# Kernel optimization log

Hardware: AMD Instinct MI355X
Metric: run time of the kernel (lower is better)

## Reference

```python
import jax, jax.numpy as jnp
import numpy as np


def setup_inputs() -> dict:
    key = jax.random.key(0)
    ks = jax.random.split(key, 9)
    bs, nf, h, w = 4, 512, 64, 64
    c8 = nf // 8
    sc = 1.0 / np.sqrt(nf)
    return {
        "x": jax.random.normal(ks[0], (bs, nf, h, w), dtype=jnp.float32),
        "Wq": jax.random.normal(ks[1], (c8, nf), dtype=jnp.float32) * sc,
        "bq": jax.random.normal(ks[2], (c8,), dtype=jnp.float32) * 0.01,
        "Wk": jax.random.normal(ks[3], (c8, nf), dtype=jnp.float32) * sc,
        "bk": jax.random.normal(ks[4], (c8,), dtype=jnp.float32) * 0.01,
        "Wv": jax.random.normal(ks[5], (nf, nf), dtype=jnp.float32) * sc,
        "bv": jax.random.normal(ks[6], (nf,), dtype=jnp.float32) * 0.01,
        "alpha": jax.random.normal(ks[7], (1,), dtype=jnp.float32) * 0.1,
    }


def reference(x, Wq, bq, Wk, bk, Wv, bv, alpha):
    bs, nf, h, w = x.shape
    hw = h * w
    xf = x.reshape(bs, nf, hw)  # flatten spatial; 1x1 conv == channel matmul
    q = jnp.einsum('oc,bcn->bon', Wq, xf) + bq[:, None]  # (bs, c8, hw)
    k = jnp.einsum('oc,bcn->bon', Wk, xf) + bk[:, None]  # (bs, c8, hw)
    v = jnp.einsum('oc,bcn->bon', Wv, xf) + bv[:, None]  # (bs, nf, hw)
    # scores[b, i, j] = key_i . query_j ; softmax over j (queries)
    scores = jnp.einsum('bci,bcj->bij', k, q)  # (bs, hw, hw)
    attn = jax.nn.softmax(scores, axis=-1)
    # out[b, c, i] = sum_j v[b, c, j] * attn[b, i, j]
    out = jnp.einsum('bcj,bij->bci', v, attn).reshape(bs, nf, h, w)
    return x + alpha * out
```

## Files before the change

### kernel.cpp

```cpp
#include <hip/hip_runtime.h>

#define BS 4
#define NF 512
#define HW 4096
#define C8 64
#define TI 64

typedef unsigned short bfu;
typedef __attribute__((ext_vector_type(8))) short bf16x8;
typedef __attribute__((ext_vector_type(4))) float f32x4;

static __device__ __forceinline__ bfu f2bu(float v) {
    union { unsigned int u; float f; } c; c.f = v;
    unsigned int u = c.u;
    u = u + 0x7FFFu + ((u >> 16) & 1u);
    return (bfu)(u >> 16);
}

static __device__ __forceinline__ unsigned int cvt_pk_bf16(float lo, float hi) {
    unsigned int r;
    asm("v_cvt_pk_bf16_f32 %0, %1, %2" : "=v"(r) : "v"(lo), "v"(hi));
    return r;
}

static __device__ __forceinline__ void gload16(const void* g, void* l) {
    __builtin_amdgcn_global_load_lds(
        (const __attribute__((address_space(1))) unsigned int*)g,
        (__attribute__((address_space(3))) unsigned int*)l,
        16, 0, 0);
}

__global__ __launch_bounds__(256) void k0_xt(const float* __restrict__ x, bfu* __restrict__ xt)
{
    __shared__ float T[64][68];
    const int t  = threadIdx.x;
    const int n0 = blockIdx.x * 64;
    const int c0 = blockIdx.y * 64;
    const int b  = blockIdx.z;

    #pragma unroll
    for (int u = 0; u < 4; u++) {
        int f4 = u * 256 + t;
        int cc = f4 >> 4;
        int n4 = (f4 & 15) << 2;
        float4 v = *(const float4*)(x + ((size_t)(b * NF + c0 + cc)) * HW + n0 + n4);
        *(float4*)&T[cc][n4 ^ (((cc >> 3) & 3) << 2)] = v;
    }
    __syncthreads();
    #pragma unroll
    for (int u = 0; u < 2; u++) {
        int e8 = u * 256 + t;
        int nn = e8 >> 3;
        int c8 = (e8 & 7) << 3;
        union { int4 i4; bfu h[8]; } pk;
        #pragma unroll
        for (int q = 0; q < 8; q++)
            pk.h[q] = f2bu(T[c8 + q][nn ^ ((((c8 + q) >> 3) & 3) << 2)]);
        *(int4*)(xt + ((size_t)(b * HW + n0 + nn)) * NF + c0 + c8) = pk.i4;
    }
}

__global__ __launch_bounds__(256) void k0_w(const float* __restrict__ Wq, const float* __restrict__ bq,
                                            const float* __restrict__ Wk, const float* __restrict__ bk,
                                            const float* __restrict__ Wv, const float* __restrict__ bv,
                                            bfu* __restrict__ Wb, float* __restrict__ bcat)
{
    const int o = blockIdx.x;
    const int t = threadIdx.x;
    const float* src; float bias;
    if (o < 64)       { src = Wq + (size_t)o * NF;          bias = bq[o]; }
    else if (o < 128) { src = Wk + (size_t)(o - 64) * NF;   bias = bk[o - 64]; }
    else              { src = Wv + (size_t)(o - 128) * NF;  bias = bv[o - 128]; }
    float2 v = *(const float2*)(src + t * 2);
    Wb[(size_t)o * NF + t * 2 + 0] = f2bu(v.x);
    Wb[(size_t)o * NF + t * 2 + 1] = f2bu(v.y);
    if (t == 0) bcat[o] = bias;
}

__global__ __launch_bounds__(256) void k1_proj(const bfu* __restrict__ Wb, const float* __restrict__ bcat,
                                               const bfu* __restrict__ xt,
                                               bfu* __restrict__ Qb, bfu* __restrict__ Kb, bfu* __restrict__ Vb)
{
    __shared__ bfu As[2][128 * 64];
    __shared__ bfu Bs[2][128 * 64];
    const int t  = threadIdx.x;
    const int o0 = blockIdx.x * 128;
    const int n0 = blockIdx.y * 128;
    const int b  = blockIdx.z;
    const int lane = t & 63, wv = t >> 6;
    const int wm = wv & 1, wn = wv >> 1;
    const int l15 = lane & 15, quad = lane >> 4;
    const int r7  = l15 & 7;
    const int sl0 = (quad ^ r7) * 8;
    const int sl1 = ((quad + 4) ^ r7) * 8;

    const int srow = t >> 3;
    const int scolz = ((t & 7) ^ (srow & 7)) * 8;

    const bfu* gA = Wb + ((size_t)(o0 + srow)) * NF + scolz;
    const bfu* gB = xt + ((size_t)(b * HW + n0 + srow)) * NF + scolz;

    f32x4 acc[4][4];
    #pragma unroll
    for (int m = 0; m < 4; m++)
        #pragma unroll
        for (int n = 0; n < 4; n++) acc[m][n] = (f32x4){0.f, 0.f, 0.f, 0.f};

#define K1_STAGE(buf, c0)                                                       \
    _Pragma("unroll")                                                           \
    for (int p = 0; p < 4; p++) {                                               \
        gload16(gA + (size_t)(p * 32) * NF + (c0), &As[buf][t * 8 + p * 2048]); \
        gload16(gB + (size_t)(p * 32) * NF + (c0), &Bs[buf][t * 8 + p * 2048]); \
    }

#define K1_COMPUTE(pc)                                                                      \
    {                                                                                       \
        bf16x8 Af0[4], Af1[4], Bf0[4], Bf1[4];                                              \
        _Pragma("unroll")                                                                   \
        for (int m = 0; m < 4; m++) {                                                       \
            const bfu* ar = &As[pc][(wm * 64 + m * 16 + l15) * 64];                         \
            Af0[m] = *(const bf16x8*)(ar + sl0);                                            \
            Af1[m] = *(const bf16x8*)(ar + sl1);                                            \
        }                                                                                   \
        _Pragma("unroll")                                                                   \
        for (int n = 0; n < 4; n++) {                                                       \
            const bfu* br = &Bs[pc][(wn * 64 + n * 16 + l15) * 64];                         \
            Bf0[n] = *(const bf16x8*)(br + sl0);                                            \
            Bf1[n] = *(const bf16x8*)(br + sl1);                                            \
        }                                                                                   \
        __builtin_amdgcn_s_setprio(1);                                                      \
        _Pragma("unroll")                                                                   \
        for (int m = 0; m < 4; m++)                                                         \
            _Pragma("unroll")                                                               \
            for (int n = 0; n < 4; n++) {                                                   \
                acc[m][n] = __builtin_amdgcn_mfma_f32_16x16x32_bf16(Af0[m], Bf0[n], acc[m][n], 0, 0, 0); \
                acc[m][n] = __builtin_amdgcn_mfma_f32_16x16x32_bf16(Af1[m], Bf1[n], acc[m][n], 0, 0, 0); \
            }                                                                               \
        __builtin_amdgcn_s_setprio(0);                                                      \
    }

    K1_STAGE(0, 0)
    for (int it = 0; it < 7; it++) {
        const int pc = it & 1;
        K1_STAGE(pc ^ 1, (it + 1) * 64)
        asm volatile("s_waitcnt vmcnt(8)" ::: "memory");
        __builtin_amdgcn_sched_barrier(0);
        __builtin_amdgcn_s_barrier();
        K1_COMPUTE(pc)
        __builtin_amdgcn_sched_barrier(0);
        __builtin_amdgcn_s_barrier();
    }
    asm volatile("s_waitcnt vmcnt(0)" ::: "memory");
    __builtin_amdgcn_sched_barrier(0);
    __builtin_amdgcn_s_barrier();
    K1_COMPUTE(1)
#undef K1_STAGE
#undef K1_COMPUTE

    if (o0 == 0) {
        #pragma unroll
        for (int mt = 0; mt < 4; mt++)
            #pragma unroll
            for (int nt = 0; nt < 4; nt++) {
                int goq = wm * 64 + mt * 16 + quad * 4;
                int n   = n0 + wn * 64 + nt * 16 + l15;
                float v0 = acc[mt][nt][0] + bcat[goq + 0];
                float v1 = acc[mt][nt][1] + bcat[goq + 1];
                float v2 = acc[mt][nt][2] + bcat[goq + 2];
                float v3 = acc[mt][nt][3] + bcat[goq + 3];
                int2 pk;
                pk.x = (int)cvt_pk_bf16(v0, v1);
                pk.y = (int)cvt_pk_bf16(v2, v3);
                if (wm == 0) *(int2*)(Qb + ((size_t)(b * HW + n)) * C8 + goq)      = pk;
                else         *(int2*)(Kb + ((size_t)(b * HW + n)) * C8 + goq - 64) = pk;
            }
    } else {
        #pragma unroll
        for (int mt = 0; mt < 4; mt++)
            #pragma unroll
            for (int nt = 0; nt < 4; nt++)
                #pragma unroll
                for (int r = 0; r < 4; r++) {
                    int go = o0 + wm * 64 + mt * 16 + quad * 4 + r;
                    int n  = n0 + wn * 64 + nt * 16 + l15;
                    float val = acc[mt][nt][r] + bcat[go];
                    Vb[((size_t)(b * NF + (go - 128))) * HW + n] = f2bu(val);
                }
    }
}

__global__ __launch_bounds__(512, 4) void k23_fused(const bfu* __restrict__ Kb, const bfu* __restrict__ Qb,
                                                    const bfu* __restrict__ Vb,
                                                    const float* __restrict__ x, const float* __restrict__ alpha,
                                                    float* __restrict__ out)
{
    __shared__ bfu   Vs[2][256 * 64];
    __shared__ bfu   Ps[TI * 72];
    __shared__ float LSum[8][2][16];
    __shared__ float Scale[TI];

    const int t = threadIdx.x;
    const int lane = t & 63, w = t >> 6;
    const int l15 = lane & 15, quad = lane >> 4;
    const int jq  = w & 3;
    const int iqb = (w >> 2) * 32;

    const int d    = blockIdx.x;
    const int xcd  = d & 7;
    const int b    = xcd >> 1;
    const int cblk = xcd & 1;
    const int i0   = (d >> 3) * TI;

    const bfu* kp0 = Kb + ((size_t)(b * HW + i0 + iqb + l15)) * C8 + quad * 8;
    const bfu* kp1 = kp0 + (size_t)16 * C8;
    const bf16x8 Kf00 = *(const bf16x8*)kp0;
    const bf16x8 Kf01 = *(const bf16x8*)(kp0 + 32);
    const bf16x8 Kf10 = *(const bf16x8*)kp1;
    const bf16x8 Kf11 = *(const bf16x8*)(kp1 + 32);

    const int srow = t >> 3, sslot = t & 7;
    const bfu* gV = Vb + ((size_t)(b * NF + cblk * 256 + srow)) * HW + ((sslot ^ (srow & 7)) * 8);

    const bfu* qbase = Qb + ((size_t)(b * HW + jq * 16 + l15)) * C8 + quad * 8;

    const int r7  = l15 & 7;
    const int sl0 = (quad ^ r7) * 8;
    const int sl1 = ((quad + 4) ^ r7) * 8;

    f32x4 acc[2][4];
    #pragma unroll
    for (int mt = 0; mt < 2; mt++)
        #pragma unroll
        for (int nt = 0; nt < 4; nt++) acc[mt][nt] = (f32x4){0.f, 0.f, 0.f, 0.f};
    float rs0 = 0.f, rs1 = 0.f;
    bf16x8 Aq[2][2];

    {
        #pragma unroll
        for (int p = 0; p < 4; p++)
            gload16(gV + (size_t)(p * 64) * HW, &Vs[0][t * 8 + p * 4096]);
        Aq[0][0] = *(const bf16x8*)qbase;
        Aq[0][1] = *(const bf16x8*)(qbase + 32);
    }

#define K23_ITER(q, pc, pn)                                                                    \
  {                                                                                            \
    const int jn = (((q) + 1) & 63) * 64;                                                      \
                          \
    _Pragma("unroll")                                                                          \
    for (int p = 0; p < 4; p++)                                                                \
        gload16(gV + (size_t)(p * 64) * HW + jn, &Vs[pn][t * 8 + p * 4096]);                   \
    {                                                                                          \
        const bfu* qpn = qbase + (size_t)jn * C8;                                              \
        Aq[pn][0] = *(const bf16x8*)qpn;                                                       \
        Aq[pn][1] = *(const bf16x8*)(qpn + 32);                                                \
    }                                                                                          \
        \
    asm volatile("s_waitcnt vmcnt(6)" ::: "memory");                                           \
    __builtin_amdgcn_sched_barrier(0);                                                         \
                                    \
    {                                                                                          \
        f32x4 s0 = (f32x4){0.f,0.f,0.f,0.f}, s1 = (f32x4){0.f,0.f,0.f,0.f};                    \
        s0 = __builtin_amdgcn_mfma_f32_16x16x32_bf16(Aq[pc][0], Kf00, s0, 0, 0, 0);            \
        s0 = __builtin_amdgcn_mfma_f32_16x16x32_bf16(Aq[pc][1], Kf01, s0, 0, 0, 0);            \
        s1 = __builtin_amdgcn_mfma_f32_16x16x32_bf16(Aq[pc][0], Kf10, s1, 0, 0, 0);            \
        s1 = __builtin_amdgcn_mfma_f32_16x16x32_bf16(Aq[pc][1], Kf11, s1, 0, 0, 0);            \
        float e0 = __expf(s0[0]), e1 = __expf(s0[1]), e2 = __expf(s0[2]), e3 = __expf(s0[3]);  \
        float f0 = __expf(s1[0]), f1 = __expf(s1[1]), f2 = __expf(s1[2]), f3 = __expf(s1[3]);  \
        rs0 += (e0 + e1) + (e2 + e3);                                                          \
        rs1 += (f0 + f1) + (f2 + f3);                                                          \
        uint2 pk0, pk1;                                                                        \
        pk0.x = cvt_pk_bf16(e0, e1);  pk0.y = cvt_pk_bf16(e2, e3);                             \
        pk1.x = cvt_pk_bf16(f0, f1);  pk1.y = cvt_pk_bf16(f2, f3);                             \
        *(uint2*)(Ps + (iqb + l15)      * 72 + jq * 16 + quad * 4) = pk0;                      \
        *(uint2*)(Ps + (iqb + 16 + l15) * 72 + jq * 16 + quad * 4) = pk1;                      \
    }                                                                                          \
    asm volatile("s_waitcnt lgkmcnt(0)" ::: "memory");                                         \
    __builtin_amdgcn_sched_barrier(0);                                                         \
    __builtin_amdgcn_s_barrier();                       \
                                               \
    {                                                                                          \
        bf16x8 Pf[4][2];                                                                       \
        _Pragma("unroll")                                                                      \
        for (int nt = 0; nt < 4; nt++) {                                                       \
            Pf[nt][0] = *(const bf16x8*)(Ps + (nt * 16 + l15) * 72 + quad * 8);                \
            Pf[nt][1] = *(const bf16x8*)(Ps + (nt * 16 + l15) * 72 + 32 + quad * 8);           \
        }                                                                                      \
        __builtin_amdgcn_s_setprio(1);                                                         \
        _Pragma("unroll")                                                                      \
        for (int mt = 0; mt < 2; mt++) {                                                       \
            const bfu* vrow = &Vs[pc][(w * 32 + mt * 16 + l15) * 64];                          \
            bf16x8 V0 = *(const bf16x8*)(vrow + sl0);                                          \
            bf16x8 V1 = *(const bf16x8*)(vrow + sl1);                                          \
            _Pragma("unroll")                                                                  \
            for (int nt = 0; nt < 4; nt++) {                                                   \
                acc[mt][nt] = __builtin_amdgcn_mfma_f32_16x16x32_bf16(V0, Pf[nt][0], acc[mt][nt], 0, 0, 0); \
                acc[mt][nt] = __builtin_amdgcn_mfma_f32_16x16x32_bf16(V1, Pf[nt][1], acc[mt][nt], 0, 0, 0); \
            }                                                                                  \
        }                                                                                      \
        __builtin_amdgcn_s_setprio(0);                                                         \
    }                                                                                          \
    __builtin_amdgcn_sched_barrier(0);                                                         \
    __builtin_amdgcn_s_barrier();    \
  }

    for (int qq = 0; qq < 32; qq++) {
        K23_ITER(2 * qq,     0, 1)
        K23_ITER(2 * qq + 1, 1, 0)
    }
#undef K23_ITER

    float sred0 = rs0, sred1 = rs1;
    sred0 += __shfl_xor(sred0, 16, 64);
    sred0 += __shfl_xor(sred0, 32, 64);
    sred1 += __shfl_xor(sred1, 16, 64);
    sred1 += __shfl_xor(sred1, 32, 64);
    if (quad == 0) { LSum[w][0][l15] = sred0; LSum[w][1][l15] = sred1; }
    __syncthreads();
    if (t < TI) {
        int u = t >> 5, s = (t >> 4) & 1, il = t & 15;
        float L = (LSum[u * 4 + 0][s][il] + LSum[u * 4 + 1][s][il])
                + (LSum[u * 4 + 2][s][il] + LSum[u * 4 + 3][s][il]);
        Scale[t] = alpha[0] / L;
    }
    __syncthreads();

    #pragma unroll
    for (int nt = 0; nt < 4; nt++) {
        float sc = Scale[nt * 16 + l15];
        int i = i0 + nt * 16 + l15;
        #pragma unroll
        for (int mt = 0; mt < 2; mt++)
            #pragma unroll
            for (int r = 0; r < 4; r++) {
                int c = cblk * 256 + w * 32 + mt * 16 + quad * 4 + r;
                size_t idx = ((size_t)(b * NF + c)) * HW + i;
                out[idx] = x[idx] + sc * acc[mt][nt][r];
            }
    }
}

extern "C" void kernel_launch(void* const* d_in, const int* in_sizes, int n_in,
                              void* d_out, int out_size, void* d_ws, size_t ws_size,
                              hipStream_t stream)
{
    const float* x     = (const float*)d_in[0];
    const float* Wq    = (const float*)d_in[1];
    const float* bq    = (const float*)d_in[2];
    const float* Wk    = (const float*)d_in[3];
    const float* bk    = (const float*)d_in[4];
    const float* Wv    = (const float*)d_in[5];
    const float* bv    = (const float*)d_in[6];
    const float* alpha = (const float*)d_in[7];
    float* out = (float*)d_out;

    char* ws = (char*)d_ws;
    bfu*   xt   = (bfu*)(ws);
    bfu*   Wb   = (bfu*)(ws + (16u << 20));
    float* bcat = (float*)(ws + (17u << 20));
    bfu*   Qb   = (bfu*)(ws + (18u << 20));
    bfu*   Kb   = (bfu*)(ws + (20u << 20));
    bfu*   Vb   = (bfu*)(ws + (22u << 20));

    k0_xt<<<dim3(HW / 64, NF / 64, BS), 256, 0, stream>>>(x, xt);
    k0_w<<<dim3(640), 256, 0, stream>>>(Wq, bq, Wk, bk, Wv, bv, Wb, bcat);
    k1_proj<<<dim3(5, HW / 128, BS), 256, 0, stream>>>(Wb, bcat, xt, Qb, Kb, Vb);
    k23_fused<<<dim3(HW / TI * BS * 2), 512, 0, stream>>>(Kb, Qb, Vb, x, alpha, out);
}
```

Measured before the change: 240.6 us.

## Cover all channels per block with smaller key chunks to avoid recomputing scores

```diff
diff --git a/kernel.cpp b/kernel.cpp
--- a/kernel.cpp
+++ b/kernel.cpp
@@ -5,6 +5,7 @@
 #define HW 4096
 #define C8 64
 #define TI 64
+#define JC 32
 
 typedef unsigned short bfu;
 typedef __attribute__((ext_vector_type(8))) short bf16x8;
@@ -194,109 +195,91 @@
                                                     const float* __restrict__ x, const float* __restrict__ alpha,
                                                     float* __restrict__ out)
 {
-    __shared__ bfu   Vs[2][256 * 64];
-    __shared__ bfu   Ps[TI * 72];
-    __shared__ float LSum[8][2][16];
+    __shared__ bfu   Vs[2][512 * JC];
+    __shared__ bfu   Ps[TI * 40];
+    __shared__ float LSum[8][16];
     __shared__ float Scale[TI];
 
     const int t = threadIdx.x;
     const int lane = t & 63, w = t >> 6;
     const int l15 = lane & 15, quad = lane >> 4;
-    const int jq  = w & 3;
-    const int iqb = (w >> 2) * 32;
+    const int iq = w >> 1, jq = w & 1;
+    const int cw = w * 64;
 
     const int d    = blockIdx.x;
     const int xcd  = d & 7;
     const int b    = xcd >> 1;
-    const int cblk = xcd & 1;
-    const int i0   = (d >> 3) * TI;
-
-    const bfu* kp0 = Kb + ((size_t)(b * HW + i0 + iqb + l15)) * C8 + quad * 8;
-    const bfu* kp1 = kp0 + (size_t)16 * C8;
-    const bf16x8 Kf00 = *(const bf16x8*)kp0;
-    const bf16x8 Kf01 = *(const bf16x8*)(kp0 + 32);
-    const bf16x8 Kf10 = *(const bf16x8*)kp1;
-    const bf16x8 Kf11 = *(const bf16x8*)(kp1 + 32);
-
-    const int srow = t >> 3, sslot = t & 7;
-    const bfu* gV = Vb + ((size_t)(b * NF + cblk * 256 + srow)) * HW + ((sslot ^ (srow & 7)) * 8);
+    const int i0   = ((xcd & 1) * 32 + (d >> 3)) * TI;
+
+    const bfu* kp = Kb + ((size_t)(b * HW + i0 + iq * 16 + l15)) * C8 + quad * 8;
+    const bf16x8 Kf0 = *(const bf16x8*)kp;
+    const bf16x8 Kf1 = *(const bf16x8*)(kp + 32);
+
+    const int srow = t >> 2;
+    const bfu* gV = Vb + ((size_t)(b * NF + srow)) * HW + (((t & 3) ^ ((t >> 3) & 3)) * 8);
 
     const bfu* qbase = Qb + ((size_t)(b * HW + jq * 16 + l15)) * C8 + quad * 8;
 
-    const int r7  = l15 & 7;
-    const int sl0 = (quad ^ r7) * 8;
-    const int sl1 = ((quad + 4) ^ r7) * 8;
-
-    f32x4 acc[2][4];
-    #pragma unroll
-    for (int mt = 0; mt < 2; mt++)
+    const int vsl = (quad ^ ((l15 >> 1) & 3)) * 8;
+
+    f32x4 acc[4][4];
+    #pragma unroll
+    for (int mt = 0; mt < 4; mt++)
         #pragma unroll
         for (int nt = 0; nt < 4; nt++) acc[mt][nt] = (f32x4){0.f, 0.f, 0.f, 0.f};
-    float rs0 = 0.f, rs1 = 0.f;
+    float rs = 0.f;
     bf16x8 Aq[2][2];
 
     {
         #pragma unroll
         for (int p = 0; p < 4; p++)
-            gload16(gV + (size_t)(p * 64) * HW, &Vs[0][t * 8 + p * 4096]);
+            gload16(gV + (size_t)(p * 128) * HW, &Vs[0][t * 8 + p * 4096]);
         Aq[0][0] = *(const bf16x8*)qbase;
         Aq[0][1] = *(const bf16x8*)(qbase + 32);
     }
 
 #define K23_ITER(q, pc, pn)                                                                    \
   {                                                                                            \
-    const int jn = (((q) + 1) & 63) * 64;                                                      \
+    const int jn = (((q) + 1) & 127) * JC;                                                     \
                           \
     _Pragma("unroll")                                                                          \
     for (int p = 0; p < 4; p++)                                                                \
-        gload16(gV + (size_t)(p * 64) * HW + jn, &Vs[pn][t * 8 + p * 4096]);                   \
+        gload16(gV + (size_t)(p * 128) * HW + jn, &Vs[pn][t * 8 + p * 4096]);                  \
     {                                                                                          \
         const bfu* qpn = qbase + (size_t)jn * C8;                                              \
         Aq[pn][0] = *(const bf16x8*)qpn;                                                       \
         Aq[pn][1] = *(const bf16x8*)(qpn + 32);                                                \
     }                                                                                          \
-        \
+               \
     asm volatile("s_waitcnt vmcnt(6)" ::: "memory");                                           \
     __builtin_amdgcn_sched_barrier(0);                                                         \
-                                    \
+                                      \
     {                                                                                          \
-        f32x4 s0 = (f32x4){0.f,0.f,0.f,0.f}, s1 = (f32x4){0.f,0.f,0.f,0.f};                    \
-        s0 = __builtin_amdgcn_mfma_f32_16x16x32_bf16(Aq[pc][0], Kf00, s0, 0, 0, 0);            \
-        s0 = __builtin_amdgcn_mfma_f32_16x16x32_bf16(Aq[pc][1], Kf01, s0, 0, 0, 0);            \
-        s1 = __builtin_amdgcn_mfma_f32_16x16x32_bf16(Aq[pc][0], Kf10, s1, 0, 0, 0);            \
-        s1 = __builtin_amdgcn_mfma_f32_16x16x32_bf16(Aq[pc][1], Kf11, s1, 0, 0, 0);            \
-        float e0 = __expf(s0[0]), e1 = __expf(s0[1]), e2 = __expf(s0[2]), e3 = __expf(s0[3]);  \
-        float f0 = __expf(s1[0]), f1 = __expf(s1[1]), f2 = __expf(s1[2]), f3 = __expf(s1[3]);  \
-        rs0 += (e0 + e1) + (e2 + e3);                                                          \
-        rs1 += (f0 + f1) + (f2 + f3);                                                          \
-        uint2 pk0, pk1;                                                                        \
-        pk0.x = cvt_pk_bf16(e0, e1);  pk0.y = cvt_pk_bf16(e2, e3);                             \
-        pk1.x = cvt_pk_bf16(f0, f1);  pk1.y = cvt_pk_bf16(f2, f3);                             \
-        *(uint2*)(Ps + (iqb + l15)      * 72 + jq * 16 + quad * 4) = pk0;                      \
-        *(uint2*)(Ps + (iqb + 16 + l15) * 72 + jq * 16 + quad * 4) = pk1;                      \
+        f32x4 s = (f32x4){0.f,0.f,0.f,0.f};                                                    \
+        s = __builtin_amdgcn_mfma_f32_16x16x32_bf16(Aq[pc][0], Kf0, s, 0, 0, 0);               \
+        s = __builtin_amdgcn_mfma_f32_16x16x32_bf16(Aq[pc][1], Kf1, s, 0, 0, 0);               \
+        float e0 = __expf(s[0]), e1 = __expf(s[1]), e2 = __expf(s[2]), e3 = __expf(s[3]);      \
+        rs += (e0 + e1) + (e2 + e3);                                                           \
+        uint2 pk;                                                                              \
+        pk.x = cvt_pk_bf16(e0, e1);  pk.y = cvt_pk_bf16(e2, e3);                               \
+        *(uint2*)(Ps + (iq * 16 + l15) * 40 + jq * 16 + quad * 4) = pk;                        \
     }                                                                                          \
     asm volatile("s_waitcnt lgkmcnt(0)" ::: "memory");                                         \
     __builtin_amdgcn_sched_barrier(0);                                                         \
     __builtin_amdgcn_s_barrier();                       \
-                                               \
+                      \
     {                                                                                          \
-        bf16x8 Pf[4][2];                                                                       \
+        bf16x8 Pf[4];                                                                          \
         _Pragma("unroll")                                                                      \
-        for (int nt = 0; nt < 4; nt++) {                                                       \
-            Pf[nt][0] = *(const bf16x8*)(Ps + (nt * 16 + l15) * 72 + quad * 8);                \
-            Pf[nt][1] = *(const bf16x8*)(Ps + (nt * 16 + l15) * 72 + 32 + quad * 8);           \
-        }                                                                                      \
+        for (int nt = 0; nt < 4; nt++)                                                         \
+            Pf[nt] = *(const bf16x8*)(Ps + (nt * 16 + l15) * 40 + quad * 8);                   \
         __builtin_amdgcn_s_setprio(1);                                                         \
         _Pragma("unroll")                                                                      \
-        for (int mt = 0; mt < 2; mt++) {                                                       \
-            const bfu* vrow = &Vs[pc][(w * 32 + mt * 16 + l15) * 64];                          \
-            bf16x8 V0 = *(const bf16x8*)(vrow + sl0);                                          \
-            bf16x8 V1 = *(const bf16x8*)(vrow + sl1);                                          \
+        for (int mt = 0; mt < 4; mt++) {                                                       \
+            const bf16x8 Vf = *(const bf16x8*)(&Vs[pc][(cw + mt * 16 + l15) * JC] + vsl);      \
             _Pragma("unroll")                                                                  \
-            for (int nt = 0; nt < 4; nt++) {                                                   \
-                acc[mt][nt] = __builtin_amdgcn_mfma_f32_16x16x32_bf16(V0, Pf[nt][0], acc[mt][nt], 0, 0, 0); \
-                acc[mt][nt] = __builtin_amdgcn_mfma_f32_16x16x32_bf16(V1, Pf[nt][1], acc[mt][nt], 0, 0, 0); \
-            }                                                                                  \
+            for (int nt = 0; nt < 4; nt++)                                                     \
+                acc[mt][nt] = __builtin_amdgcn_mfma_f32_16x16x32_bf16(Vf, Pf[nt], acc[mt][nt], 0, 0, 0); \
         }                                                                                      \
         __builtin_amdgcn_s_setprio(0);                                                         \
     }                                                                                          \
@@ -304,23 +287,20 @@
     __builtin_amdgcn_s_barrier();    \
   }
 
-    for (int qq = 0; qq < 32; qq++) {
+    for (int qq = 0; qq < 64; qq++) {
         K23_ITER(2 * qq,     0, 1)
         K23_ITER(2 * qq + 1, 1, 0)
     }
 #undef K23_ITER
 
-    float sred0 = rs0, sred1 = rs1;
-    sred0 += __shfl_xor(sred0, 16, 64);
-    sred0 += __shfl_xor(sred0, 32, 64);
-    sred1 += __shfl_xor(sred1, 16, 64);
-    sred1 += __shfl_xor(sred1, 32, 64);
-    if (quad == 0) { LSum[w][0][l15] = sred0; LSum[w][1][l15] = sred1; }
+    float sred = rs;
+    sred += __shfl_xor(sred, 16, 64);
+    sred += __shfl_xor(sred, 32, 64);
+    if (quad == 0) LSum[w][l15] = sred;
     __syncthreads();
     if (t < TI) {
-        int u = t >> 5, s = (t >> 4) & 1, il = t & 15;
-        float L = (LSum[u * 4 + 0][s][il] + LSum[u * 4 + 1][s][il])
-                + (LSum[u * 4 + 2][s][il] + LSum[u * 4 + 3][s][il]);
+        int iqq = t >> 4, il = t & 15;
+        float L = LSum[iqq * 2 + 0][il] + LSum[iqq * 2 + 1][il];
         Scale[t] = alpha[0] / L;
     }
     __syncthreads();
@@ -330,10 +310,10 @@
         float sc = Scale[nt * 16 + l15];
         int i = i0 + nt * 16 + l15;
         #pragma unroll
-        for (int mt = 0; mt < 2; mt++)
+        for (int mt = 0; mt < 4; mt++)
             #pragma unroll
             for (int r = 0; r < 4; r++) {
-                int c = cblk * 256 + w * 32 + mt * 16 + quad * 4 + r;
+                int c = cw + mt * 16 + quad * 4 + r;
                 size_t idx = ((size_t)(b * NF + c)) * HW + i;
                 out[idx] = x[idx] + sc * acc[mt][nt][r];
             }
@@ -365,5 +345,5 @@
     k0_xt<<<dim3(HW / 64, NF / 64, BS), 256, 0, stream>>>(x, xt);
     k0_w<<<dim3(640), 256, 0, stream>>>(Wq, bq, Wk, bk, Wv, bv, Wb, bcat);
     k1_proj<<<dim3(5, HW / 128, BS), 256, 0, stream>>>(Wb, bcat, xt, Qb, Kb, Vb);
-    k23_fused<<<dim3(HW / TI * BS * 2), 512, 0, stream>>>(Kb, Qb, Vb, x, alpha, out);
-}
+    k23_fused<<<dim3(HW / TI * BS), 512, 0, stream>>>(Kb, Qb, Vb, x, alpha, out);
+}
```

After: 285.0 us. 18.5% more time.

## Software-pipeline score/exp ahead of PV MFMA, swizzle P tile, merge prep kernels

Applied to the files above, without the earlier changes.

```diff
diff --git a/kernel.cpp b/kernel.cpp
--- a/kernel.cpp
+++ b/kernel.cpp
@@ -5,6 +5,7 @@
 #define HW 4096
 #define C8 64
 #define TI 64
+#define JC 64
 
 typedef unsigned short bfu;
 typedef __attribute__((ext_vector_type(8))) short bf16x8;
@@ -30,13 +31,32 @@
         16, 0, 0);
 }
 
-__global__ __launch_bounds__(256) void k0_xt(const float* __restrict__ x, bfu* __restrict__ xt)
+__global__ __launch_bounds__(256) void k0_pre(const float* __restrict__ x, bfu* __restrict__ xt,
+                                              const float* __restrict__ Wq, const float* __restrict__ bq,
+                                              const float* __restrict__ Wk, const float* __restrict__ bk,
+                                              const float* __restrict__ Wv, const float* __restrict__ bv,
+                                              bfu* __restrict__ Wb, float* __restrict__ bcat)
 {
     __shared__ float T[64][68];
-    const int t  = threadIdx.x;
-    const int n0 = blockIdx.x * 64;
-    const int c0 = blockIdx.y * 64;
-    const int b  = blockIdx.z;
+    const int t   = threadIdx.x;
+    const int bid = blockIdx.x;
+
+    if (bid >= 2048) {
+        const int o = bid - 2048;
+        const float* src; float bias;
+        if (o < 64)       { src = Wq + (size_t)o * NF;          bias = bq[o]; }
+        else if (o < 128) { src = Wk + (size_t)(o - 64) * NF;   bias = bk[o - 64]; }
+        else              { src = Wv + (size_t)(o - 128) * NF;  bias = bv[o - 128]; }
+        float2 v = *(const float2*)(src + t * 2);
+        Wb[(size_t)o * NF + t * 2 + 0] = f2bu(v.x);
+        Wb[(size_t)o * NF + t * 2 + 1] = f2bu(v.y);
+        if (t == 0) bcat[o] = bias;
+        return;
+    }
+
+    const int n0 = (bid & 63) * 64;
+    const int c0 = ((bid >> 6) & 7) * 64;
+    const int b  = bid >> 9;
 
     #pragma unroll
     for (int u = 0; u < 4; u++) {
@@ -58,23 +78,6 @@
             pk.h[q] = f2bu(T[c8 + q][nn ^ ((((c8 + q) >> 3) & 3) << 2)]);
         *(int4*)(xt + ((size_t)(b * HW + n0 + nn)) * NF + c0 + c8) = pk.i4;
     }
-}
-
-__global__ __launch_bounds__(256) void k0_w(const float* __restrict__ Wq, const float* __restrict__ bq,
-                                            const float* __restrict__ Wk, const float* __restrict__ bk,
-                                            const float* __restrict__ Wv, const float* __restrict__ bv,
-                                            bfu* __restrict__ Wb, float* __restrict__ bcat)
-{
-    const int o = blockIdx.x;
-    const int t = threadIdx.x;
-    const float* src; float bias;
-    if (o < 64)       { src = Wq + (size_t)o * NF;          bias = bq[o]; }
-    else if (o < 128) { src = Wk + (size_t)(o - 64) * NF;   bias = bk[o - 64]; }
-    else              { src = Wv + (size_t)(o - 128) * NF;  bias = bv[o - 128]; }
-    float2 v = *(const float2*)(src + t * 2);
-    Wb[(size_t)o * NF + t * 2 + 0] = f2bu(v.x);
-    Wb[(size_t)o * NF + t * 2 + 1] = f2bu(v.y);
-    if (t == 0) bcat[o] = bias;
 }
 
 __global__ __launch_bounds__(256) void k1_proj(const bfu* __restrict__ Wb, const float* __restrict__ bcat,
@@ -195,7 +198,7 @@
                                                     float* __restrict__ out)
 {
     __shared__ bfu   Vs[2][256 * 64];
-    __shared__ bfu   Ps[TI * 72];
+    __shared__ bfu   Ps[64 * 64];
     __shared__ float LSum[8][2][16];
     __shared__ float Scale[TI];
 
@@ -226,6 +229,7 @@
     const int r7  = l15 & 7;
     const int sl0 = (quad ^ r7) * 8;
     const int sl1 = ((quad + 4) ^ r7) * 8;
+    const int pwz = ((jq * 2 + (quad >> 1)) ^ r7) * 8 + (quad & 1) * 4;
 
     f32x4 acc[2][4];
     #pragma unroll
@@ -235,36 +239,80 @@
     float rs0 = 0.f, rs1 = 0.f;
     bf16x8 Aq[2][2];
 
+    Aq[0][0] = *(const bf16x8*)qbase;
+    Aq[0][1] = *(const bf16x8*)(qbase + 32);
+    #pragma unroll
+    for (int p = 0; p < 4; p++)
+        gload16(gV + (size_t)(p * 64) * HW, &Vs[0][t * 8 + p * 4096]);
     {
-        #pragma unroll
-        for (int p = 0; p < 4; p++)
-            gload16(gV + (size_t)(p * 64) * HW, &Vs[0][t * 8 + p * 4096]);
-        Aq[0][0] = *(const bf16x8*)qbase;
-        Aq[0][1] = *(const bf16x8*)(qbase + 32);
+        f32x4 s0 = (f32x4){0.f,0.f,0.f,0.f}, s1 = (f32x4){0.f,0.f,0.f,0.f};
+        s0 = __builtin_amdgcn_mfma_f32_16x16x32_bf16(Aq[0][0], Kf00, s0, 0, 0, 0);
+        s0 = __builtin_amdgcn_mfma_f32_16x16x32_bf16(Aq[0][1], Kf01, s0, 0, 0, 0);
+        s1 = __builtin_amdgcn_mfma_f32_16x16x32_bf16(Aq[0][0], Kf10, s1, 0, 0, 0);
+        s1 = __builtin_amdgcn_mfma_f32_16x16x32_bf16(Aq[0][1], Kf11, s1, 0, 0, 0);
+        float e0 = __expf(s0[0]), e1 = __expf(s0[1]), e2 = __expf(s0[2]), e3 = __expf(s0[3]);
+        float f0 = __expf(s1[0]), f1 = __expf(s1[1]), f2 = __expf(s1[2]), f3 = __expf(s1[3]);
+        rs0 += (e0 + e1) + (e2 + e3);
+        rs1 += (f0 + f1) + (f2 + f3);
+        uint2 pk0, pk1;
+        pk0.x = cvt_pk_bf16(e0, e1);  pk0.y = cvt_pk_bf16(e2, e3);
+        pk1.x = cvt_pk_bf16(f0, f1);  pk1.y = cvt_pk_bf16(f2, f3);
+        *(uint2*)(Ps + (iqb + l15)      * 64 + pwz) = pk0;
+        *(uint2*)(Ps + (iqb + 16 + l15) * 64 + pwz) = pk1;
     }
 
 #define K23_ITER(q, pc, pn)                                                                    \
   {                                                                                            \
-    const int jn = (((q) + 1) & 63) * 64;                                                      \
-                          \
-    _Pragma("unroll")                                                                          \
-    for (int p = 0; p < 4; p++)                                                                \
-        gload16(gV + (size_t)(p * 64) * HW + jn, &Vs[pn][t * 8 + p * 4096]);                   \
+    const int jn = (((q) + 1) & 63) * JC;                                                      \
+                                      \
     {                                                                                          \
         const bfu* qpn = qbase + (size_t)jn * C8;                                              \
         Aq[pn][0] = *(const bf16x8*)qpn;                                                       \
         Aq[pn][1] = *(const bf16x8*)(qpn + 32);                                                \
     }                                                                                          \
-        \
-    asm volatile("s_waitcnt vmcnt(6)" ::: "memory");                                           \
+    _Pragma("unroll")                                                                          \
+    for (int p = 0; p < 4; p++)                                                                \
+        gload16(gV + (size_t)(p * 64) * HW + jn, &Vs[pn][t * 8 + p * 4096]);                   \
+             \
+    asm volatile("s_waitcnt vmcnt(6) lgkmcnt(0)" ::: "memory");                                \
     __builtin_amdgcn_sched_barrier(0);                                                         \
-                                    \
+    __builtin_amdgcn_s_barrier();                        \
+                    \
+    f32x4 s0 = (f32x4){0.f,0.f,0.f,0.f}, s1 = (f32x4){0.f,0.f,0.f,0.f};                        \
+    if (jn) {                                                                                  \
+        s0 = __builtin_amdgcn_mfma_f32_16x16x32_bf16(Aq[pn][0], Kf00, s0, 0, 0, 0);            \
+        s0 = __builtin_amdgcn_mfma_f32_16x16x32_bf16(Aq[pn][1], Kf01, s0, 0, 0, 0);            \
+        s1 = __builtin_amdgcn_mfma_f32_16x16x32_bf16(Aq[pn][0], Kf10, s1, 0, 0, 0);            \
+        s1 = __builtin_amdgcn_mfma_f32_16x16x32_bf16(Aq[pn][1], Kf11, s1, 0, 0, 0);            \
+    }                                                                                          \
+                                     \
     {                                                                                          \
-        f32x4 s0 = (f32x4){0.f,0.f,0.f,0.f}, s1 = (f32x4){0.f,0.f,0.f,0.f};                    \
-        s0 = __builtin_amdgcn_mfma_f32_16x16x32_bf16(Aq[pc][0], Kf00, s0, 0, 0, 0);            \
-        s0 = __builtin_amdgcn_mfma_f32_16x16x32_bf16(Aq[pc][1], Kf01, s0, 0, 0, 0);            \
-        s1 = __builtin_amdgcn_mfma_f32_16x16x32_bf16(Aq[pc][0], Kf10, s1, 0, 0, 0);            \
-        s1 = __builtin_amdgcn_mfma_f32_16x16x32_bf16(Aq[pc][1], Kf11, s1, 0, 0, 0);            \
+        bf16x8 V0[2], V1[2];                                                                   \
+        _Pragma("unroll")                                                                      \
+        for (int mt = 0; mt < 2; mt++) {                                                       \
+            const bfu* vrow = &Vs[pc][(w * 32 + mt * 16 + l15) * 64];                          \
+            V0[mt] = *(const bf16x8*)(vrow + sl0);                                             \
+            V1[mt] = *(const bf16x8*)(vrow + sl1);                                             \
+        }                                                                                      \
+        __builtin_amdgcn_s_setprio(1);                                                         \
+        _Pragma("unroll")                                                                      \
+        for (int nt = 0; nt < 4; nt++) {                                                       \
+            const bfu* prow = Ps + (nt * 16 + l15) * 64;                                       \
+            bf16x8 Pf0 = *(const bf16x8*)(prow + sl0);                                         \
+            bf16x8 Pf1 = *(const bf16x8*)(prow + sl1);                                         \
+            _Pragma("unroll")                                                                  \
+            for (int mt = 0; mt < 2; mt++) {                                                   \
+                acc[mt][nt] = __builtin_amdgcn_mfma_f32_16x16x32_bf16(V0[mt], Pf0, acc[mt][nt], 0, 0, 0); \
+                acc[mt][nt] = __builtin_amdgcn_mfma_f32_16x16x32_bf16(V1[mt], Pf1, acc[mt][nt], 0, 0, 0); \
+            }                                                                                  \
+        }                                                                                      \
+        __builtin_amdgcn_s_setprio(0);                                                         \
+    }                                                                                          \
+    asm volatile("s_waitcnt lgkmcnt(0)" ::: "memory");                                         \
+    __builtin_amdgcn_sched_barrier(0);                                                         \
+    __builtin_amdgcn_s_barrier();        \
+                                 \
+    if (jn) {                                                                                  \
         float e0 = __expf(s0[0]), e1 = __expf(s0[1]), e2 = __expf(s0[2]), e3 = __expf(s0[3]);  \
         float f0 = __expf(s1[0]), f1 = __expf(s1[1]), f2 = __expf(s1[2]), f3 = __expf(s1[3]);  \
         rs0 += (e0 + e1) + (e2 + e3);                                                          \
@@ -272,36 +320,9 @@
         uint2 pk0, pk1;                                                                        \
         pk0.x = cvt_pk_bf16(e0, e1);  pk0.y = cvt_pk_bf16(e2, e3);                             \
         pk1.x = cvt_pk_bf16(f0, f1);  pk1.y = cvt_pk_bf16(f2, f3);                             \
-        *(uint2*)(Ps + (iqb + l15)      * 72 + jq * 16 + quad * 4) = pk0;                      \
-        *(uint2*)(Ps + (iqb + 16 + l15) * 72 + jq * 16 + quad * 4) = pk1;                      \
+        *(uint2*)(Ps + (iqb + l15)      * 64 + pwz) = pk0;                                     \
+        *(uint2*)(Ps + (iqb + 16 + l15) * 64 + pwz) = pk1;                                     \
     }                                                                                          \
-    asm volatile("s_waitcnt lgkmcnt(0)" ::: "memory");                                         \
-    __builtin_amdgcn_sched_barrier(0);                                                         \
-    __builtin_amdgcn_s_barrier();                       \
-                                               \
-    {                                                                                          \
-        bf16x8 Pf[4][2];                                                                       \
-        _Pragma("unroll")                                                                      \
-        for (int nt = 0; nt < 4; nt++) {                                                       \
-            Pf[nt][0] = *(const bf16x8*)(Ps + (nt * 16 + l15) * 72 + quad * 8);                \
-            Pf[nt][1] = *(const bf16x8*)(Ps + (nt * 16 + l15) * 72 + 32 + quad * 8);           \
-        }                                                                                      \
-        __builtin_amdgcn_s_setprio(1);                                                         \
-        _Pragma("unroll")                                                                      \
-        for (int mt = 0; mt < 2; mt++) {                                                       \
-            const bfu* vrow = &Vs[pc][(w * 32 + mt * 16 + l15) * 64];                          \
-            bf16x8 V0 = *(const bf16x8*)(vrow + sl0);                                          \
-            bf16x8 V1 = *(const bf16x8*)(vrow + sl1);                                          \
-            _Pragma("unroll")                                                                  \
-            for (int nt = 0; nt < 4; nt++) {                                                   \
-                acc[mt][nt] = __builtin_amdgcn_mfma_f32_16x16x32_bf16(V0, Pf[nt][0], acc[mt][nt], 0, 0, 0); \
-                acc[mt][nt] = __builtin_amdgcn_mfma_f32_16x16x32_bf16(V1, Pf[nt][1], acc[mt][nt], 0, 0, 0); \
-            }                                                                                  \
-        }                                                                                      \
-        __builtin_amdgcn_s_setprio(0);                                                         \
-    }                                                                                          \
-    __builtin_amdgcn_sched_barrier(0);                                                         \
-    __builtin_amdgcn_s_barrier();    \
   }
 
     for (int qq = 0; qq < 32; qq++) {
@@ -362,8 +383,7 @@
     bfu*   Kb   = (bfu*)(ws + (20u << 20));
     bfu*   Vb   = (bfu*)(ws + (22u << 20));
 
-    k0_xt<<<dim3(HW / 64, NF / 64, BS), 256, 0, stream>>>(x, xt);
-    k0_w<<<dim3(640), 256, 0, stream>>>(Wq, bq, Wk, bk, Wv, bv, Wb, bcat);
+    k0_pre<<<dim3(2048 + 640), 256, 0, stream>>>(x, xt, Wq, bq, Wk, bk, Wv, bv, Wb, bcat);
     k1_proj<<<dim3(5, HW / 128, BS), 256, 0, stream>>>(Wb, bcat, xt, Qb, Kb, Vb);
     k23_fused<<<dim3(HW / TI * BS * 2), 512, 0, stream>>>(Kb, Qb, Vb, x, alpha, out);
 }
```

New measurement: 218.8 us. 9.0% less time.
